# Performance work log

Measured on AMD Instinct MI355X. Metric: run time of the kernel, lower is better.

## Reference

```python
import jax, jax.numpy as jnp
import numpy as np

# Forest of B perfect binary trees, depth D levels, M = 2**D - 1 nodes/tree.
B, D, H, X, VOCAB, NCLS = 32, 12, 256, 256, 32000, 20
M = 2 ** D - 1          # 4095 nodes per tree
N = B * M               # 131040 total nodes


def setup_inputs() -> dict:
    key = jax.random.key(0)
    ks = jax.random.split(key, 9)
    x = jax.random.randint(ks[0], (N,), 0, VOCAB, dtype=jnp.int32)
    # leaves are the last level of each tree: in-tree index >= 2**(D-1)-1
    leaf = (jnp.arange(M) >= 2 ** (D - 1) - 1).astype(jnp.int32)
    x_mask = jnp.tile(leaf, B)  # [N] int32, 1 on leaves, 0 on internal nodes
    s = 0.02
    Emb = jax.random.normal(ks[1], (VOCAB, X), jnp.float32) * s
    W_iou = jax.random.normal(ks[2], (3 * H, X), jnp.float32) * s
    b_iou = jnp.zeros((3 * H,), jnp.float32)
    U_iou = jax.random.normal(ks[3], (3 * H, H), jnp.float32) * s
    U_f = jax.random.normal(ks[4], (H, H), jnp.float32) * s
    b_f = jnp.ones((H,), jnp.float32)  # forget-gate bias init
    W_out = jax.random.normal(ks[5], (NCLS, H), jnp.float32) * s
    b_out = jnp.zeros((NCLS,), jnp.float32)
    return {"x": x, "x_mask": x_mask, "Emb": Emb, "W_iou": W_iou,
            "b_iou": b_iou, "U_iou": U_iou, "U_f": U_f, "b_f": b_f,
            "W_out": W_out, "b_out": b_out}


def reference(x, x_mask, Emb, W_iou, b_iou, U_iou, U_f, b_f, W_out, b_out):
    # input_module: embedding applied to masked ids, result masked again
    x_emb = Emb[x * x_mask] * x_mask[:, None].astype(Emb.dtype)      # [N, X]
    xiou = (x_emb @ W_iou.T).reshape(B, M, 3 * H)                    # W_iou * x per node
    h_sum = jnp.zeros((B, M, H), Emb.dtype)    # sum of children h (childsum)
    fc_sum = jnp.zeros((B, M, H), Emb.dtype)   # sum_k f_k * c_k from children
    h_all = jnp.zeros((B, M, H), Emb.dtype)
    # topological propagation: leaves (deepest level) -> roots
    for l in range(D - 1, -1, -1):
        s_, e_ = 2 ** l - 1, 2 ** (l + 1) - 1  # static in-tree level slice
        iou = xiou[:, s_:e_] + h_sum[:, s_:e_] @ U_iou.T + b_iou
        i, o, u = jnp.split(iou, 3, axis=-1)
        c = jax.nn.sigmoid(i) * jnp.tanh(u) + fc_sum[:, s_:e_]
        h = jax.nn.sigmoid(o) * jnp.tanh(c)
        h_all = h_all.at[:, s_:e_].set(h)
        if l > 0:
            f = jax.nn.sigmoid(h @ U_f.T + b_f)          # per-child forget gate
            parents = (np.arange(s_, e_) - 1) // 2       # static parent indices
            h_sum = h_sum.at[:, parents].add(h)
            fc_sum = fc_sum.at[:, parents].add(f * c)
    # output_module applied to all node states
    return h_all.reshape(N, H) @ W_out.T + b_out                    # [N, NCLS]
```

## Files before the change

### kernel.cpp

```cpp
#include <hip/hip_runtime.h>

#define B_TREES 32
#define DEPTH   12
#define M_NODES 4095
#define N_NODES (B_TREES * M_NODES)
#define HDIM    256
#define VOCAB   32000
#define NCLS    20
#define LEAFROWS 65536
#define LDSH_S 20

typedef _Float16 f16;
typedef _Float16 f16x8 __attribute__((ext_vector_type(8)));
typedef _Float16 f16x4 __attribute__((ext_vector_type(4)));
typedef _Float16 f16x2 __attribute__((ext_vector_type(2)));
typedef float    f32x4 __attribute__((ext_vector_type(4)));

__device__ __forceinline__ float sigf(float x)      { return 1.0f / (1.0f + __expf(-x)); }
__device__ __forceinline__ float tanh_fast(float x) { return 1.0f - 2.0f / (1.0f + __expf(2.0f * x)); }

__global__ __launch_bounds__(256) void cvt_kernel(
    const float4* __restrict__ Emb,  const float4* __restrict__ Wiou,
    const float4* __restrict__ Uiou, const float4* __restrict__ Uf,
    const float4* __restrict__ Wout,
    f16x4* __restrict__ Emb16,  f16x4* __restrict__ Wiou16,
    f16x4* __restrict__ Uiou16, f16x4* __restrict__ Uf16,
    f16x4* __restrict__ Wout16)
{
    int i = blockIdx.x * 256 + threadIdx.x;
    if (i < VOCAB * HDIM / 4) {
        float4 v = Emb[i];
        f16x4 r; r[0] = (f16)v.x; r[1] = (f16)v.y; r[2] = (f16)v.z; r[3] = (f16)v.w;
        Emb16[i] = r;
    }
    if (i < 768 * HDIM / 4) {
        float4 v = Wiou[i];
        f16x4 r; r[0] = (f16)v.x; r[1] = (f16)v.y; r[2] = (f16)v.z; r[3] = (f16)v.w;
        Wiou16[i] = r;
        float4 u = Uiou[i];
        f16x4 s; s[0] = (f16)u.x; s[1] = (f16)u.y; s[2] = (f16)u.z; s[3] = (f16)u.w;
        Uiou16[i] = s;
    }
    if (i < HDIM * HDIM / 4) {
        float4 v = Uf[i];
        f16x4 r; r[0] = (f16)v.x; r[1] = (f16)v.y; r[2] = (f16)v.z; r[3] = (f16)v.w;
        Uf16[i] = r;
    }
    if (i < 32 * HDIM / 4) {
        int row = i >> 6;
        f16x4 r = {};
        if (row < NCLS) {
            float4 v = Wout[i];
            r[0] = (f16)v.x; r[1] = (f16)v.y; r[2] = (f16)v.z; r[3] = (f16)v.w;
        }
        Wout16[i] = r;
    }
}

#define VTPW 5
__global__ __launch_bounds__(256) void vocab_kernel(
    const f16* __restrict__ Emb16, const f16* __restrict__ Wiou16,
    const float* __restrict__ b_iou,
    f16* __restrict__ hv, f16* __restrict__ cv)
{
    __shared__ f16 wlds[1536 * 8];
    __shared__ f16 ldshH[4][16 * LDSH_S];
    __shared__ f16 ldshC[4][16 * LDSH_S];

    const int tid  = threadIdx.x;
    const int lane = tid & 63;
    const int w    = tid >> 6;
    const int quad = lane >> 4;
    const int l15  = lane & 15;
    const int qk   = quad * 8;
    const int cb0  = blockIdx.y * 16;

    #pragma unroll
    for (int i = 0; i < 6; ++i) {
        int f = i * 256 + tid;
        int mat = f >> 9, r = f & 511, ks = r >> 6, q = (r >> 4) & 3, c = r & 15;
        *(f16x8*)(wlds + f * 8) = *(const f16x8*)(Wiou16 +
            (mat * 256 + cb0 + c) * HDIM + ks * 32 + q * 8);
    }
    __syncthreads();

    const float bi = b_iou[cb0 + l15];
    const float bo = b_iou[256 + cb0 + l15];
    const float bu = b_iou[512 + cb0 + l15];

    const int row0 = (blockIdx.x * 4 + w) * (VTPW * 16);

    f16x8 a[8];
    #pragma unroll
    for (int ks = 0; ks < 8; ++ks)
        a[ks] = *(const f16x8*)(Emb16 + (row0 + l15) * HDIM + ks * 32 + qk);

    for (int rt = 0; rt < VTPW; ++rt) {
        const int rw = row0 + rt * 16;
        f16x8 ac[8];
        #pragma unroll
        for (int ks = 0; ks < 8; ++ks) ac[ks] = a[ks];

        if (rt + 1 < VTPW) {
            #pragma unroll
            for (int ks = 0; ks < 8; ++ks)
                a[ks] = *(const f16x8*)(Emb16 + (rw + 16 + l15) * HDIM + ks * 32 + qk);
        }

        f32x4 acc[3] = {};
        #pragma unroll
        for (int ks = 0; ks < 8; ++ks) {
            #pragma unroll
            for (int mat = 0; mat < 3; ++mat) {
                f16x8 wf = *(const f16x8*)(wlds +
                    ((mat * 8 + ks) * 64 + quad * 16 + l15) * 8);
                acc[mat] = __builtin_amdgcn_mfma_f32_16x16x32_f16(
                    ac[ks], wf, acc[mat], 0, 0, 0);
            }
        }

        #pragma unroll
        for (int r = 0; r < 4; ++r) {
            float i_ = acc[0][r] + bi;
            float o_ = acc[1][r] + bo;
            float u_ = acc[2][r] + bu;
            float c  = sigf(i_) * tanh_fast(u_);
            float h  = sigf(o_) * tanh_fast(c);
            ldshH[w][(quad * 4 + r) * LDSH_S + l15] = (f16)h;
            ldshC[w][(quad * 4 + r) * LDSH_S + l15] = (f16)c;
        }

        {
            int row_l = lane >> 2, cpos = (lane & 3) * 4;
            f16x4 vh = *(const f16x4*)(&ldshH[w][row_l * LDSH_S + cpos]);
            *(f16x4*)(hv + (rw + row_l) * HDIM + cb0 + cpos) = vh;
            f16x4 vc = *(const f16x4*)(&ldshC[w][row_l * LDSH_S + cpos]);
            *(f16x4*)(cv + (rw + row_l) * HDIM + cb0 + cpos) = vc;
        }
    }
}

__global__ __launch_bounds__(256) void vocab_out_kernel(
    const f16* __restrict__ hv, const f16* __restrict__ Wout16,
    const float* __restrict__ bout, float* __restrict__ out_v)
{
    const int lane = threadIdx.x & 63;
    const int w    = threadIdx.x >> 6;
    const int quad = lane >> 4;
    const int l15  = lane & 15;
    const int qk   = quad * 8;

    f16x8 wfk[2][8];
    #pragma unroll
    for (int cf = 0; cf < 2; ++cf)
        #pragma unroll
        for (int ks = 0; ks < 8; ++ks)
            wfk[cf][ks] = *(const f16x8*)(Wout16 +
                (cf * 16 + l15) * HDIM + ks * 32 + qk);
    float bo[2];
    #pragma unroll
    for (int cf = 0; cf < 2; ++cf) {
        int col = cf * 16 + l15;
        bo[cf] = bout[col < NCLS ? col : 0];
    }

    const int tile0 = blockIdx.x * 16;

    for (int rt = w; rt < 16; rt += 4) {
        const int rw = (tile0 + rt) * 16;
        f32x4 acc[2] = {};
        #pragma unroll
        for (int ks = 0; ks < 8; ++ks) {
            f16x8 a = *(const f16x8*)(hv + (rw + l15) * HDIM + ks * 32 + qk);
            #pragma unroll
            for (int cf = 0; cf < 2; ++cf)
                acc[cf] = __builtin_amdgcn_mfma_f32_16x16x32_f16(
                    a, wfk[cf][ks], acc[cf], 0, 0, 0);
        }
        #pragma unroll
        for (int cf = 0; cf < 2; ++cf) {
            const int col = cf * 16 + l15;
            if (col < NCLS) {
                #pragma unroll
                for (int r = 0; r < 4; ++r)
                    out_v[(rw + quad * 4 + r) * NCLS + col] = acc[cf][r] + bo[cf];
            }
        }
    }
}

__global__ __launch_bounds__(256) void leaf_scatter_kernel(
    const int* __restrict__ x, const f16* __restrict__ hv,
    const f16* __restrict__ cv, const float* __restrict__ out_v,
    f16* __restrict__ h16, f16* __restrict__ cT, float* __restrict__ out)
{
    __shared__ int ids[64];
    __shared__ f16 ldsc[64][HDIM + 8];

    const int tid = threadIdx.x;
    const int R0  = blockIdx.x * 64;

    if (tid < 64) {
        int r = R0 + tid;
        int node = (r >> 11) * M_NODES + 2047 + (r & 2047);
        ids[tid] = x[node];
    }
    __syncthreads();

    const int r    = tid >> 2;
    const int p    = tid & 3;
    const int id   = ids[r];
    const int gr   = R0 + r;
    const int node = (gr >> 11) * M_NODES + 2047 + (gr & 2047);

    #pragma unroll
    for (int j = 0; j < 8; ++j) {
        f16x8 v = *(const f16x8*)(hv + id * HDIM + p * 64 + j * 8);
        *(f16x8*)(h16 + node * HDIM + p * 64 + j * 8) = v;
    }
    #pragma unroll
    for (int j = 0; j < 8; ++j) {
        f16x8 v = *(const f16x8*)(cv + id * HDIM + p * 64 + j * 8);
        *(f16x8*)(&ldsc[r][p * 64 + j * 8]) = v;
    }
    #pragma unroll
    for (int j = 0; j < 5; ++j)
        out[node * NCLS + p * 5 + j] = out_v[id * NCLS + p * 5 + j];

    __syncthreads();

    {
        const int c = tid;
        f16 tmp[64];
        #pragma unroll
        for (int rr = 0; rr < 64; ++rr) tmp[rr] = ldsc[rr][c];
        #pragma unroll
        for (int j = 0; j < 8; ++j)
            *(f16x8*)(cT + c * LEAFROWS + R0 + j * 8) = *(const f16x8*)(&tmp[j * 8]);
    }
}

__global__ __launch_bounds__(512) void fused_level_kernel(
    const f16* __restrict__ Uiou16, const f16* __restrict__ Uf16,
    const float* __restrict__ b_iou, const float* __restrict__ b_f,
    f16* __restrict__ h16, const f16* __restrict__ cT_child,
    f16* __restrict__ cT_parent, int l, int rows_p, int tpw)
{
    __shared__ f16 wlds[2048 * 8];
    __shared__ f16 ldsh[8][16 * LDSH_S];

    const int tid  = threadIdx.x;
    const int lane = tid & 63;
    const int w    = tid >> 6;
    const int quad = lane >> 4;
    const int l15  = lane & 15;
    const int qk   = quad * 8;
    const int cb0  = blockIdx.y * 16;

    #pragma unroll
    for (int i = 0; i < 4; ++i) {
        int f = i * 512 + tid;
        int mat = f >> 9, r = f & 511, ks = r >> 6, q = (r >> 4) & 3, c = r & 15;
        const f16* src = (mat == 0)
            ? (Uf16 + (cb0 + c) * HDIM + ks * 32 + q * 8)
            : (Uiou16 + ((mat - 1) * 256 + cb0 + c) * HDIM + ks * 32 + q * 8);
        *(f16x8*)(wlds + f * 8) = *(const f16x8*)src;
    }
    __syncthreads();

    const float bi  = b_iou[cb0 + l15];
    const float bo  = b_iou[256 + cb0 + l15];
    const float bu  = b_iou[512 + cb0 + l15];
    const float bfv = b_f[cb0 + l15];
    const int lc = l + 1;
    const int maskc = (1 << lc) - 1;
    const int maskp = (1 << l) - 1;
    const int rows_c = rows_p * 2;

    const int p0 = blockIdx.x * (tpw * 128);

    for (int pt = 0; pt < tpw; ++pt) {
        const int pw = p0 + (pt * 8 + w) * 16;
        if (pw >= rows_p) continue;
        const int cw = 2 * pw;

        int childBase0, childBase1;
        {
            int cl0 = cw + l15;
            childBase0 = ((cl0 >> lc) * M_NODES + maskc + (cl0 & maskc)) * HDIM;
            int cl1 = cw + 16 + l15;
            childBase1 = ((cl1 >> lc) * M_NODES + maskc + (cl1 & maskc)) * HDIM;
        }

        f32x4 accf0 = {}, accf1 = {};
        f32x4 au0[3] = {}, au1[3] = {};
        #pragma unroll
        for (int ks = 0; ks < 8; ++ks) {
            const int k0 = ks * 32 + qk;
            f16x8 a0 = *(const f16x8*)(h16 + childBase0 + k0);
            f16x8 a1 = *(const f16x8*)(h16 + childBase1 + k0);
            f16x8 wfF = *(const f16x8*)(wlds + (ks * 64 + quad * 16 + l15) * 8);
            accf0 = __builtin_amdgcn_mfma_f32_16x16x32_f16(a0, wfF, accf0, 0, 0, 0);
            accf1 = __builtin_amdgcn_mfma_f32_16x16x32_f16(a1, wfF, accf1, 0, 0, 0);
            #pragma unroll
            for (int m = 0; m < 3; ++m) {
                f16x8 wm = *(const f16x8*)(wlds +
                    (((m + 1) * 8 + ks) * 64 + quad * 16 + l15) * 8);
                au0[m] = __builtin_amdgcn_mfma_f32_16x16x32_f16(a0, wm, au0[m], 0, 0, 0);
                au1[m] = __builtin_amdgcn_mfma_f32_16x16x32_f16(a1, wm, au1[m], 0, 0, 0);
            }
        }

        #pragma unroll
        for (int s = 0; s < 2; ++s) {
            const f32x4& af = s ? accf1 : accf0;
            const f32x4* au = s ? au1 : au0;
            const int csr = cw + s * 16;
            f16x4 cc = *(const f16x4*)(cT_child +
                (cb0 + l15) * rows_c + csr + quad * 4);
            f16x2 cpack;
            #pragma unroll
            for (int pr = 0; pr < 2; ++pr) {
                float f0 = sigf(af[2 * pr]     + bfv);
                float f1 = sigf(af[2 * pr + 1] + bfv);
                float fc = f0 * (float)cc[2 * pr] + f1 * (float)cc[2 * pr + 1];
                float i_ = au[0][2 * pr] + au[0][2 * pr + 1] + bi;
                float o_ = au[1][2 * pr] + au[1][2 * pr + 1] + bo;
                float u_ = au[2][2 * pr] + au[2][2 * pr + 1] + bu;
                float c  = sigf(i_) * tanh_fast(u_) + fc;
                float h  = sigf(o_) * tanh_fast(c);
                cpack[pr] = (f16)c;
                ldsh[w][(s * 8 + quad * 2 + pr) * LDSH_S + l15] = (f16)h;
            }
            *(f16x2*)(cT_parent + (cb0 + l15) * rows_p + pw + s * 8 + quad * 2) = cpack;
        }

        {
            int prow = lane >> 2, cpos = (lane & 3) * 4;
            int p = pw + prow;
            int b = p >> l, tt = p & maskp;
            int node = b * M_NODES + (1 << l) - 1 + tt;
            f16x4 v = *(const f16x4*)(&ldsh[w][prow * LDSH_S + cpos]);
            *(f16x4*)(h16 + node * HDIM + cb0 + cpos) = v;
        }
    }
}

__global__ __launch_bounds__(256) void out_kernel(
    const f16* __restrict__ h16, const f16* __restrict__ Wout16,
    const float* __restrict__ bout, float* __restrict__ out)
{
    const int lane = threadIdx.x & 63;
    const int w    = threadIdx.x >> 6;
    const int quad = lane >> 4;
    const int l15  = lane & 15;
    const int qk   = quad * 8;

    f16x8 wfk[2][8];
    #pragma unroll
    for (int cf = 0; cf < 2; ++cf)
        #pragma unroll
        for (int ks = 0; ks < 8; ++ks)
            wfk[cf][ks] = *(const f16x8*)(Wout16 +
                (cf * 16 + l15) * HDIM + ks * 32 + qk);
    float bo[2];
    #pragma unroll
    for (int cf = 0; cf < 2; ++cf) {
        int col = cf * 16 + l15;
        bo[cf] = bout[col < NCLS ? col : 0];
    }

    const int tile0 = blockIdx.x * 16;

    for (int rt = w; rt < 16; rt += 4) {
        const int tt = tile0 + rt;
        const int rw = (tt >> 7) * M_NODES + (tt & 127) * 16;
        f32x4 acc[2] = {};
        #pragma unroll
        for (int ks = 0; ks < 8; ++ks) {
            f16x8 a = *(const f16x8*)(h16 + (rw + l15) * HDIM + ks * 32 + qk);
            #pragma unroll
            for (int cf = 0; cf < 2; ++cf)
                acc[cf] = __builtin_amdgcn_mfma_f32_16x16x32_f16(
                    a, wfk[cf][ks], acc[cf], 0, 0, 0);
        }
        #pragma unroll
        for (int cf = 0; cf < 2; ++cf) {
            const int col = cf * 16 + l15;
            if (col < NCLS) {
                #pragma unroll
                for (int r = 0; r < 4; ++r)
                    out[(rw + quad * 4 + r) * NCLS + col] = acc[cf][r] + bo[cf];
            }
        }
    }
}

extern "C" void kernel_launch(void* const* d_in, const int* in_sizes, int n_in,
                              void* d_out, int out_size, void* d_ws, size_t ws_size,
                              hipStream_t stream)
{
    const int*   x     = (const int*)d_in[0];
    const float* Emb   = (const float*)d_in[2];
    const float* W_iou = (const float*)d_in[3];
    const float* b_iou = (const float*)d_in[4];
    const float* U_iou = (const float*)d_in[5];
    const float* U_f   = (const float*)d_in[6];
    const float* b_f   = (const float*)d_in[7];
    const float* W_out = (const float*)d_in[8];
    const float* b_out = (const float*)d_in[9];
    float* out = (float*)d_out;

    char* ws = (char*)d_ws;
    size_t off = 0;
    auto take = [&](size_t bytes) -> char* {
        char* p = ws + off; off += (bytes + 255) & ~(size_t)255; return p;
    };
    f16* h16    = (f16*)take((size_t)N_NODES * HDIM * 2);
    f16* cA     = (f16*)take((size_t)HDIM * LEAFROWS * 2);
    f16* cB     = (f16*)take((size_t)HDIM * (LEAFROWS / 2) * 2);
    f16* Emb16  = (f16*)take((size_t)VOCAB * HDIM * 2);
    f16* Wiou16 = (f16*)take((size_t)768 * HDIM * 2);
    f16* Uiou16 = (f16*)take((size_t)768 * HDIM * 2);
    f16* Uf16   = (f16*)take((size_t)HDIM * HDIM * 2);
    f16* Wout16 = (f16*)take((size_t)32 * HDIM * 2);
    f16* cv     = (f16*)take((size_t)VOCAB * HDIM * 2);
    float* outv = (float*)take((size_t)VOCAB * NCLS * 4);
    f16* hv     = cB;

    cvt_kernel<<<VOCAB * HDIM / 4 / 256, 256, 0, stream>>>(
        (const float4*)Emb, (const float4*)W_iou, (const float4*)U_iou,
        (const float4*)U_f, (const float4*)W_out,
        (f16x4*)Emb16, (f16x4*)Wiou16, (f16x4*)Uiou16, (f16x4*)Uf16,
        (f16x4*)Wout16);

    vocab_kernel<<<dim3(VOCAB / (4 * 16 * VTPW), 16), 256, 0, stream>>>(
        Emb16, Wiou16, b_iou, hv, cv);

    vocab_out_kernel<<<dim3(VOCAB / 16 / 16), 256, 0, stream>>>(
        hv, Wout16, b_out, outv);

    leaf_scatter_kernel<<<dim3(LEAFROWS / 64), 256, 0, stream>>>(
        x, hv, cv, outv, h16, cA, out);

    f16* cin  = cA;
    f16* cout_ = cB;
    for (int l = 10; l >= 0; --l) {
        int rows_p = B_TREES << l;
        int tpw = (rows_p >= 16384) ? 2 : 1;
        int gx  = (rows_p + tpw * 128 - 1) / (tpw * 128);
        fused_level_kernel<<<dim3(gx, 16), 512, 0, stream>>>(
            Uiou16, Uf16, b_iou, b_f, h16, cin, cout_, l, rows_p, tpw);
        f16* t = cin; cin = cout_; cout_ = t;
    }

    out_kernel<<<dim3(32 * 128 / 16), 256, 0, stream>>>(
        h16, Wout16, b_out, out);
}
```

Measured before the change: 406.5 us.

## Interleave two row tiles per wave in fused level kernel for ILP

Each wave now processes two 16-row parent tiles at once instead of looping over them. Their child-h loads and MFMA chains are interleaved, and the child cell-state loads are hoisted before the matmul loop. This is meant to hide global-load and MFMA latency. Every level now uses 256 rows per block, so small levels launch fewer blocks, and inactive second tiles still run redundant MFMAs on duplicate data.

```diff
diff --git a/kernel.cpp b/kernel.cpp
--- a/kernel.cpp
+++ b/kernel.cpp
@@ -244,7 +244,7 @@
     const f16* __restrict__ Uiou16, const f16* __restrict__ Uf16,
     const float* __restrict__ b_iou, const float* __restrict__ b_f,
     f16* __restrict__ h16, const f16* __restrict__ cT_child,
-    f16* __restrict__ cT_parent, int l, int rows_p, int tpw)
+    f16* __restrict__ cT_parent, int l, int rows_p)
 {
     __shared__ f16 wlds[2048 * 8];
     __shared__ f16 ldsh[8][16 * LDSH_S];
@@ -277,67 +277,93 @@
     const int maskp = (1 << l) - 1;
     const int rows_c = rows_p * 2;
 
-    const int p0 = blockIdx.x * (tpw * 128);
-
-    for (int pt = 0; pt < tpw; ++pt) {
-        const int pw = p0 + (pt * 8 + w) * 16;
-        if (pw >= rows_p) continue;
-        const int cw = 2 * pw;
-
-        int childBase0, childBase1;
-        {
-            int cl0 = cw + l15;
-            childBase0 = ((cl0 >> lc) * M_NODES + maskc + (cl0 & maskc)) * HDIM;
-            int cl1 = cw + 16 + l15;
-            childBase1 = ((cl1 >> lc) * M_NODES + maskc + (cl1 & maskc)) * HDIM;
-        }
-
-        f32x4 accf0 = {}, accf1 = {};
-        f32x4 au0[3] = {}, au1[3] = {};
-        #pragma unroll
-        for (int ks = 0; ks < 8; ++ks) {
-            const int k0 = ks * 32 + qk;
-            f16x8 a0 = *(const f16x8*)(h16 + childBase0 + k0);
-            f16x8 a1 = *(const f16x8*)(h16 + childBase1 + k0);
-            f16x8 wfF = *(const f16x8*)(wlds + (ks * 64 + quad * 16 + l15) * 8);
-            accf0 = __builtin_amdgcn_mfma_f32_16x16x32_f16(a0, wfF, accf0, 0, 0, 0);
-            accf1 = __builtin_amdgcn_mfma_f32_16x16x32_f16(a1, wfF, accf1, 0, 0, 0);
-            #pragma unroll
-            for (int m = 0; m < 3; ++m) {
-                f16x8 wm = *(const f16x8*)(wlds +
-                    (((m + 1) * 8 + ks) * 64 + quad * 16 + l15) * 8);
-                au0[m] = __builtin_amdgcn_mfma_f32_16x16x32_f16(a0, wm, au0[m], 0, 0, 0);
-                au1[m] = __builtin_amdgcn_mfma_f32_16x16x32_f16(a1, wm, au1[m], 0, 0, 0);
+    const int p0 = blockIdx.x * 256;
+
+    int  pw[2];
+    bool act[2];
+    pw[0]  = p0 + w * 16;
+    act[0] = pw[0] < rows_p;
+    if (!act[0]) pw[0] = 0;
+    pw[1]  = pw[0] + 128;
+    act[1] = act[0] && (pw[1] < rows_p);
+    if (!act[1]) pw[1] = pw[0];
+
+    int cbse[2][2];
+    #pragma unroll
+    for (int t = 0; t < 2; ++t) {
+        int cw  = 2 * pw[t];
+        int cl0 = cw + l15;
+        cbse[t][0] = ((cl0 >> lc) * M_NODES + maskc + (cl0 & maskc)) * HDIM;
+        int cl1 = cw + 16 + l15;
+        cbse[t][1] = ((cl1 >> lc) * M_NODES + maskc + (cl1 & maskc)) * HDIM;
+    }
+
+    f16x4 ccv[2][2];
+    #pragma unroll
+    for (int t = 0; t < 2; ++t)
+        #pragma unroll
+        for (int s = 0; s < 2; ++s)
+            ccv[t][s] = *(const f16x4*)(cT_child +
+                (cb0 + l15) * rows_c + 2 * pw[t] + s * 16 + quad * 4);
+
+    f32x4 accf[2][2] = {};
+    f32x4 au[2][2][3] = {};
+    #pragma unroll
+    for (int ks = 0; ks < 8; ++ks) {
+        const int k0 = ks * 32 + qk;
+        f16x8 a[2][2];
+        #pragma unroll
+        for (int t = 0; t < 2; ++t) {
+            a[t][0] = *(const f16x8*)(h16 + cbse[t][0] + k0);
+            a[t][1] = *(const f16x8*)(h16 + cbse[t][1] + k0);
+        }
+        f16x8 wfF = *(const f16x8*)(wlds + (ks * 64 + quad * 16 + l15) * 8);
+        #pragma unroll
+        for (int t = 0; t < 2; ++t) {
+            accf[t][0] = __builtin_amdgcn_mfma_f32_16x16x32_f16(a[t][0], wfF, accf[t][0], 0, 0, 0);
+            accf[t][1] = __builtin_amdgcn_mfma_f32_16x16x32_f16(a[t][1], wfF, accf[t][1], 0, 0, 0);
+        }
+        #pragma unroll
+        for (int m = 0; m < 3; ++m) {
+            f16x8 wm = *(const f16x8*)(wlds +
+                (((m + 1) * 8 + ks) * 64 + quad * 16 + l15) * 8);
+            #pragma unroll
+            for (int t = 0; t < 2; ++t) {
+                au[t][0][m] = __builtin_amdgcn_mfma_f32_16x16x32_f16(a[t][0], wm, au[t][0][m], 0, 0, 0);
+                au[t][1][m] = __builtin_amdgcn_mfma_f32_16x16x32_f16(a[t][1], wm, au[t][1][m], 0, 0, 0);
             }
         }
-
+    }
+
+    #pragma unroll
+    for (int t = 0; t < 2; ++t) {
+        if (!act[t]) continue;
+        const int pwt = pw[t];
         #pragma unroll
         for (int s = 0; s < 2; ++s) {
-            const f32x4& af = s ? accf1 : accf0;
-            const f32x4* au = s ? au1 : au0;
-            const int csr = cw + s * 16;
-            f16x4 cc = *(const f16x4*)(cT_child +
-                (cb0 + l15) * rows_c + csr + quad * 4);
+            const f32x4& af = accf[t][s];
+            const f32x4* auv = au[t][s];
+            f16x4 cc = ccv[t][s];
             f16x2 cpack;
             #pragma unroll
             for (int pr = 0; pr < 2; ++pr) {
                 float f0 = sigf(af[2 * pr]     + bfv);
                 float f1 = sigf(af[2 * pr + 1] + bfv);
                 float fc = f0 * (float)cc[2 * pr] + f1 * (float)cc[2 * pr + 1];
-                float i_ = au[0][2 * pr] + au[0][2 * pr + 1] + bi;
-                float o_ = au[1][2 * pr] + au[1][2 * pr + 1] + bo;
-                float u_ = au[2][2 * pr] + au[2][2 * pr + 1] + bu;
+                float i_ = auv[0][2 * pr] + auv[0][2 * pr + 1] + bi;
+                float o_ = auv[1][2 * pr] + auv[1][2 * pr + 1] + bo;
+                float u_ = auv[2][2 * pr] + auv[2][2 * pr + 1] + bu;
                 float c  = sigf(i_) * tanh_fast(u_) + fc;
                 float h  = sigf(o_) * tanh_fast(c);
                 cpack[pr] = (f16)c;
                 ldsh[w][(s * 8 + quad * 2 + pr) * LDSH_S + l15] = (f16)h;
             }
-            *(f16x2*)(cT_parent + (cb0 + l15) * rows_p + pw + s * 8 + quad * 2) = cpack;
+            *(f16x2*)(cT_parent + (cb0 + l15) * rows_p + pwt + s * 8 + quad * 2) = cpack;
         }
 
         {
             int prow = lane >> 2, cpos = (lane & 3) * 4;
-            int p = pw + prow;
+            int p = pwt + prow;
             int b = p >> l, tt = p & maskp;
             int node = b * M_NODES + (1 << l) - 1 + tt;
             f16x4 v = *(const f16x4*)(&ldsh[w][prow * LDSH_S + cpos]);
@@ -447,10 +473,9 @@
     f16* cout_ = cB;
     for (int l = 10; l >= 0; --l) {
         int rows_p = B_TREES << l;
-        int tpw = (rows_p >= 16384) ? 2 : 1;
-        int gx  = (rows_p + tpw * 128 - 1) / (tpw * 128);
+        int gx = (rows_p + 255) / 256;
         fused_level_kernel<<<dim3(gx, 16), 512, 0, stream>>>(
-            Uiou16, Uf16, b_iou, b_f, h16, cin, cout_, l, rows_p, tpw);
+            Uiou16, Uf16, b_iou, b_f, h16, cin, cout_, l, rows_p);
         f16* t = cin; cin = cout_; cout_ = t;
     }
 
```

Measured after the change: 471.0 us. 1.16x slower.

## Add register-resident-weight level kernel with double-buffered LDS child tiles for large levels

Applied to the files above, without the earlier changes.

Adds a new kernel for the three widest tree levels. Each wave keeps its 16-column slice of U_f and U_iou in registers, and the block streams 64-parent tiles of child h rows through a double-buffered, XOR-swizzled LDS buffer, prefetching the next tile while MFMAs run. This replaces re-staging the weights in LDS per block and uses a fixed persistent-style grid of 128x2 blocks. The cost is heavy register pressure (launch_bounds 512,2) and a large LDS footprint, which may limit occupancy. Smaller levels keep the old kernel.

```diff
diff --git a/kernel.cpp b/kernel.cpp
--- a/kernel.cpp
+++ b/kernel.cpp
@@ -240,7 +240,146 @@
     }
 }
 
-__global__ __launch_bounds__(512) void fused_level_kernel(
+__global__ __launch_bounds__(512, 2) void fused_level_big(
+    const f16* __restrict__ Uiou16, const f16* __restrict__ Uf16,
+    const float* __restrict__ b_iou, const float* __restrict__ b_f,
+    f16* __restrict__ h16, const f16* __restrict__ cT_child,
+    f16* __restrict__ cT_parent, int l, int rows_p, int nt)
+{
+    __shared__ f16 Abuf[2][32768];
+    __shared__ f16 ldsh[8][16 * LDSH_S];
+
+    const int tid  = threadIdx.x;
+    const int lane = tid & 63;
+    const int w    = tid >> 6;
+    const int quad = lane >> 4;
+    const int l15  = lane & 15;
+    const int qk   = quad * 8;
+    const int g    = blockIdx.y * 8 + w;
+    const int cb0  = g * 16;
+
+    f16x8 wfF[8], wfU[3][8];
+    #pragma unroll
+    for (int ks = 0; ks < 8; ++ks)
+        wfF[ks] = *(const f16x8*)(Uf16 + (cb0 + l15) * HDIM + ks * 32 + qk);
+    #pragma unroll
+    for (int m = 0; m < 3; ++m)
+        #pragma unroll
+        for (int ks = 0; ks < 8; ++ks)
+            wfU[m][ks] = *(const f16x8*)(Uiou16 +
+                (m * 256 + cb0 + l15) * HDIM + ks * 32 + qk);
+
+    const float bi  = b_iou[cb0 + l15];
+    const float bo  = b_iou[256 + cb0 + l15];
+    const float bu  = b_iou[512 + cb0 + l15];
+    const float bfv = b_f[cb0 + l15];
+    const int lc    = l + 1;
+    const int maskc = (1 << lc) - 1;
+    const int maskp = (1 << l) - 1;
+    const int rows_c = rows_p * 2;
+
+    const int P0base = blockIdx.x * (nt * 64);
+
+    {
+        int c0 = 2 * P0base;
+        int nb = (c0 >> lc) * M_NODES + maskc + (c0 & maskc);
+        #pragma unroll
+        for (int i = 0; i < 8; ++i) {
+            int slot = i * 512 + tid;
+            f16x8 v = *(const f16x8*)(h16 + (nb + (slot >> 5)) * HDIM + (slot & 31) * 8);
+            *(f16x8*)((char*)(&Abuf[0][0]) +
+                ((slot * 16) ^ (((slot >> 5) & 7) << 6))) = v;
+        }
+    }
+    __syncthreads();
+
+    int cur = 0;
+    for (int t = 0; t < nt; ++t) {
+        const int P0 = P0base + t * 64;
+        const bool hasNext = (t + 1 < nt);
+        int nb = 0;
+        if (hasNext) {
+            int c0 = 2 * (P0 + 64);
+            nb = (c0 >> lc) * M_NODES + maskc + (c0 & maskc);
+        }
+        const char* AbR = (const char*)(&Abuf[cur][0]);
+        char*       AbW = (char*)(&Abuf[cur ^ 1][0]);
+        const int xr = (l15 & 7) << 6;
+
+        #pragma unroll
+        for (int st = 0; st < 4; ++st) {
+            f16x8 stg0, stg1;
+            const int slot0 = st * 1024 + tid;
+            const int slot1 = slot0 + 512;
+            if (hasNext) {
+                stg0 = *(const f16x8*)(h16 + (nb + (slot0 >> 5)) * HDIM + (slot0 & 31) * 8);
+                stg1 = *(const f16x8*)(h16 + (nb + (slot1 >> 5)) * HDIM + (slot1 & 31) * 8);
+            }
+
+            const int pw = P0 + st * 16;
+            const int cw = 2 * pw;
+            f16x4 cc0 = *(const f16x4*)(cT_child + (cb0 + l15) * rows_c + cw + quad * 4);
+            f16x4 cc1 = *(const f16x4*)(cT_child + (cb0 + l15) * rows_c + cw + 16 + quad * 4);
+
+            const int rb0 = (st * 32 + l15) * 512;
+            f32x4 accf0 = {}, accf1 = {};
+            f32x4 au0[3] = {}, au1[3] = {};
+            #pragma unroll
+            for (int ks = 0; ks < 8; ++ks) {
+                const int cbyte = ks * 64 + quad * 16;
+                f16x8 a0 = *(const f16x8*)(AbR + ((rb0 + cbyte) ^ xr));
+                f16x8 a1 = *(const f16x8*)(AbR + ((rb0 + 8192 + cbyte) ^ xr));
+                accf0 = __builtin_amdgcn_mfma_f32_16x16x32_f16(a0, wfF[ks], accf0, 0, 0, 0);
+                accf1 = __builtin_amdgcn_mfma_f32_16x16x32_f16(a1, wfF[ks], accf1, 0, 0, 0);
+                #pragma unroll
+                for (int m = 0; m < 3; ++m) {
+                    au0[m] = __builtin_amdgcn_mfma_f32_16x16x32_f16(a0, wfU[m][ks], au0[m], 0, 0, 0);
+                    au1[m] = __builtin_amdgcn_mfma_f32_16x16x32_f16(a1, wfU[m][ks], au1[m], 0, 0, 0);
+                }
+            }
+
+            #pragma unroll
+            for (int s = 0; s < 2; ++s) {
+                const f32x4& af = s ? accf1 : accf0;
+                const f32x4* auv = s ? au1 : au0;
+                f16x4 cc = s ? cc1 : cc0;
+                f16x2 cpack;
+                #pragma unroll
+                for (int pr = 0; pr < 2; ++pr) {
+                    float f0 = sigf(af[2 * pr]     + bfv);
+                    float f1 = sigf(af[2 * pr + 1] + bfv);
+                    float fc = f0 * (float)cc[2 * pr] + f1 * (float)cc[2 * pr + 1];
+                    float i_ = auv[0][2 * pr] + auv[0][2 * pr + 1] + bi;
+                    float o_ = auv[1][2 * pr] + auv[1][2 * pr + 1] + bo;
+                    float u_ = auv[2][2 * pr] + auv[2][2 * pr + 1] + bu;
+                    float c  = sigf(i_) * tanh_fast(u_) + fc;
+                    float h  = sigf(o_) * tanh_fast(c);
+                    cpack[pr] = (f16)c;
+                    ldsh[w][(s * 8 + quad * 2 + pr) * LDSH_S + l15] = (f16)h;
+                }
+                *(f16x2*)(cT_parent + (cb0 + l15) * rows_p + pw + s * 8 + quad * 2) = cpack;
+            }
+
+            {
+                int prow = lane >> 2, cpos = (lane & 3) * 4;
+                int p = pw + prow;
+                int b = p >> l, tt2 = p & maskp;
+                int node = b * M_NODES + (1 << l) - 1 + tt2;
+                f16x4 v = *(const f16x4*)(&ldsh[w][prow * LDSH_S + cpos]);
+                *(f16x4*)(h16 + node * HDIM + cb0 + cpos) = v;
+            }
+
+            if (hasNext) {
+                *(f16x8*)(AbW + ((slot0 * 16) ^ (((slot0 >> 5) & 7) << 6))) = stg0;
+                *(f16x8*)(AbW + ((slot1 * 16) ^ (((slot1 >> 5) & 7) << 6))) = stg1;
+            }
+        }
+        __syncthreads();
+        cur ^= 1;
+    }
+}
+
+__global__ __launch_bounds__(512) void fused_level_small(
     const f16* __restrict__ Uiou16, const f16* __restrict__ Uf16,
     const float* __restrict__ b_iou, const float* __restrict__ b_f,
     f16* __restrict__ h16, const f16* __restrict__ cT_child,
@@ -447,10 +586,15 @@
     f16* cout_ = cB;
     for (int l = 10; l >= 0; --l) {
         int rows_p = B_TREES << l;
-        int tpw = (rows_p >= 16384) ? 2 : 1;
-        int gx  = (rows_p + tpw * 128 - 1) / (tpw * 128);
-        fused_level_kernel<<<dim3(gx, 16), 512, 0, stream>>>(
-            Uiou16, Uf16, b_iou, b_f, h16, cin, cout_, l, rows_p, tpw);
+        if (l >= 8) {
+            int nt = rows_p / 8192;
+            fused_level_big<<<dim3(128, 2), 512, 0, stream>>>(
+                Uiou16, Uf16, b_iou, b_f, h16, cin, cout_, l, rows_p, nt);
+        } else {
+            int gx = (rows_p + 127) / 128;
+            fused_level_small<<<dim3(gx, 16), 512, 0, stream>>>(
+                Uiou16, Uf16, b_iou, b_f, h16, cin, cout_, l, rows_p, 1);
+        }
         f16* t = cin; cin = cout_; cout_ = t;
     }
 
```

New measurement: 407.0 us. No clear change (+0.1%).
